# Optimization experiments

Measured on AMD Instinct MI355X. Metric: run time of the kernel, lower is better.

Reference implementation:

```python
import jax, jax.numpy as jnp
import numpy as np

NUM_TAGS = 128
BATCH = 512
SEQ = 512


def setup_inputs() -> dict:
    key = jax.random.key(0)
    k1, k2, k3, k4 = jax.random.split(key, 4)
    emissions = jax.random.normal(k1, (BATCH, SEQ, NUM_TAGS), dtype=jnp.float32)
    mask = jnp.ones((BATCH, SEQ), dtype=bool)
    start_transitions = jax.random.normal(k2, (NUM_TAGS,), dtype=jnp.float32)
    end_transitions = jax.random.normal(k3, (NUM_TAGS,), dtype=jnp.float32)
    transitions = jax.random.normal(k4, (NUM_TAGS, NUM_TAGS), dtype=jnp.float32)
    return {
        "emissions": emissions,
        "mask": mask,
        "start_transitions": start_transitions,
        "end_transitions": end_transitions,
        "transitions": transitions,
    }


def reference(emissions, mask, start_transitions, end_transitions, transitions):
    """Viterbi decode (max-plus DP + backtrace), vectorized over batch.

    Returns:
      paths:      [B, S] int32, best tag sequence; positions past seq_end are -1
      best_score: [B]    float32, Viterbi score of the best path
    """
    emissions = emissions.astype(jnp.float32)
    B, S, T = emissions.shape
    emis = jnp.swapaxes(emissions, 0, 1)   # [S, B, T]
    msk = jnp.swapaxes(mask, 0, 1)         # [S, B]

    # ---- forward max-plus recurrence ----
    score0 = start_transitions[None, :] + emis[0]        # [B, T]

    def fwd_step(score, xs):
        e_t, m_t = xs                                    # [B,T], [B]
        nxt = score[:, :, None] + transitions[None]      # [B, T_prev, T_next]
        best_score = jnp.max(nxt, axis=1) + e_t          # [B, T]
        best_tag = jnp.argmax(nxt, axis=1).astype(jnp.int32)  # [B, T]
        new_score = jnp.where(m_t[:, None], best_score, score)
        return new_score, best_tag

    score, history = jax.lax.scan(fwd_step, score0, (emis[1:], msk[1:]))
    # history: [S-1, B, T] backpointers for t = 1..S-1

    final = score + end_transitions[None, :]
    best_score = jnp.max(final, axis=1)                  # [B]
    best_last = jnp.argmax(final, axis=1).astype(jnp.int32)  # [B]

    seq_ends = jnp.sum(mask.astype(jnp.int32), axis=1) - 1   # [B]

    # ---- vectorized backtrace (reverse scan) ----
    def bwd_step(tag, xs):
        hist_t, t = xs                                   # [B,T], scalar
        path_t = tag                                     # tag at position t (valid if t <= seq_end)
        prev = jnp.take_along_axis(hist_t, tag[:, None], axis=1)[:, 0]
        tag = jnp.where(t <= seq_ends, prev, tag)
        return tag, path_t

    ts = jnp.arange(1, S)
    tag0, rev_paths = jax.lax.scan(bwd_step, best_last, (history, ts), reverse=True)
    paths = jnp.concatenate([tag0[:, None], jnp.swapaxes(rev_paths, 0, 1)], axis=1)  # [B,S]
    paths = jnp.where(mask, paths, -1)
    return paths, best_score
```

## Files before the change

kernel.cpp:

```cpp
#include <hip/hip_runtime.h>

#define NB 512
#define NS 512
#define NT 128

__global__ __launch_bounds__(512, 1)
void crf_viterbi_fast(const float* __restrict__ emis,
                      const float* __restrict__ start_t,
                      const float* __restrict__ end_t,
                      const float* __restrict__ trans,
                      float* __restrict__ out_paths,
                      float* __restrict__ out_score,
                      float* __restrict__ ws)
{
    __shared__ __align__(16) float scp[2][144];
    __shared__ float Tlds[NT * 129];
    __shared__ float finv[NT];
    __shared__ unsigned char pathb[NS];

    const int b   = blockIdx.x;
    const int tid = threadIdx.x;
    const int j   = tid >> 2;
    const int h   = tid & 3;

    for (int idx = tid; idx < NT * NT; idx += 512) {
        Tlds[(idx >> 7) * 129 + (idx & 127)] = trans[idx];
    }

    float tc[32];
    #pragma unroll
    for (int k = 0; k < 32; ++k) tc[k] = trans[(h * 32 + k) * NT + j];

    const float* eb   = emis + (size_t)b * NS * NT;
    float*       wrow = ws   + (size_t)b * NS * NT;

    const int jq = (j >> 5) * 36 + (j & 31);

    float ns = start_t[j] + eb[j];
    if (h == 0) { scp[0][jq] = ns; wrow[j] = ns; }
    __syncthreads();

    float e_next = eb[NT + j];
    int cur = 0;
    for (int t = 1; t < NS; ++t) {
        float e_cur = e_next;
        int tn = (t + 1 < NS) ? (t + 1) : (NS - 1);
        e_next = eb[(size_t)tn * NT + j];

        const float4* s4 = (const float4*)&scp[cur][h * 36];

        float m0, m1, m2, m3;
        {
            float4 A = s4[0];
            m0 = fmaxf(fmaxf(A.x + tc[0],  A.y + tc[1]),
                       fmaxf(A.z + tc[2],  A.w + tc[3]));
            A = s4[1];
            m0 = fmaxf(fmaxf(m0, A.x + tc[4]),  A.y + tc[5]);
            m0 = fmaxf(fmaxf(m0, A.z + tc[6]),  A.w + tc[7]);
            A = s4[2];
            m1 = fmaxf(fmaxf(A.x + tc[8],  A.y + tc[9]),
                       fmaxf(A.z + tc[10], A.w + tc[11]));
            A = s4[3];
            m1 = fmaxf(fmaxf(m1, A.x + tc[12]), A.y + tc[13]);
            m1 = fmaxf(fmaxf(m1, A.z + tc[14]), A.w + tc[15]);
            A = s4[4];
            m2 = fmaxf(fmaxf(A.x + tc[16], A.y + tc[17]),
                       fmaxf(A.z + tc[18], A.w + tc[19]));
            A = s4[5];
            m2 = fmaxf(fmaxf(m2, A.x + tc[20]), A.y + tc[21]);
            m2 = fmaxf(fmaxf(m2, A.z + tc[22]), A.w + tc[23]);
            A = s4[6];
            m3 = fmaxf(fmaxf(A.x + tc[24], A.y + tc[25]),
                       fmaxf(A.z + tc[26], A.w + tc[27]));
            A = s4[7];
            m3 = fmaxf(fmaxf(m3, A.x + tc[28]), A.y + tc[29]);
            m3 = fmaxf(fmaxf(m3, A.z + tc[30]), A.w + tc[31]);
        }
        float m = fmaxf(fmaxf(m0, m1), fmaxf(m2, m3));

        m = fmaxf(m, __shfl_xor(m, 1));
        m = fmaxf(m, __shfl_xor(m, 2));

        ns = m + e_cur;
        if (h == 0) {
            scp[cur ^ 1][jq] = ns;
            wrow[(size_t)t * NT + j] = ns;
        }
        __syncthreads();
        cur ^= 1;
    }

    float fin = ns + end_t[j];
    if (h == 0) finv[j] = fin;
    __syncthreads();

    if (tid < 64) {
        const int l = tid;

        float f0 = finv[l], f1 = finv[l + 64];
        float mv = fmaxf(f0, f1);
        mv = fmaxf(mv, __shfl_xor(mv, 1));
        mv = fmaxf(mv, __shfl_xor(mv, 2));
        mv = fmaxf(mv, __shfl_xor(mv, 4));
        mv = fmaxf(mv, __shfl_xor(mv, 8));
        mv = fmaxf(mv, __shfl_xor(mv, 16));
        mv = fmaxf(mv, __shfl_xor(mv, 32));
        unsigned long long b0 = __ballot(f0 == mv);
        unsigned long long b1 = __ballot(f1 == mv);
        int tag = b0 ? (int)__builtin_ctzll(b0) : 64 + (int)__builtin_ctzll(b1);
        if (l == 0) {
            out_score[b] = mv;
            pathb[NS - 1] = (unsigned char)tag;
        }

        const float* rp = wrow + (size_t)(NS - 2) * NT;
        float a0 = rp[l], a1 = rp[l + 64];

        for (int t = NS - 1; t >= 1; --t) {
            const float* rp2 = wrow + (size_t)(t >= 2 ? t - 2 : 0) * NT;
            float p0 = rp2[l], p1 = rp2[l + 64];

            float v0 = a0 + Tlds[l * 129 + tag];
            float v1 = a1 + Tlds[(l + 64) * 129 + tag];
            float m = fmaxf(v0, v1);
            m = fmaxf(m, __shfl_xor(m, 1));
            m = fmaxf(m, __shfl_xor(m, 2));
            m = fmaxf(m, __shfl_xor(m, 4));
            m = fmaxf(m, __shfl_xor(m, 8));
            m = fmaxf(m, __shfl_xor(m, 16));
            m = fmaxf(m, __shfl_xor(m, 32));
            unsigned long long c0 = __ballot(v0 == m);
            unsigned long long c1 = __ballot(v1 == m);
            tag = c0 ? (int)__builtin_ctzll(c0) : 64 + (int)__builtin_ctzll(c1);
            if (l == 0) pathb[t - 1] = (unsigned char)tag;

            a0 = p0; a1 = p1;
        }
    }
    __syncthreads();

    if (tid < NT) {
        float* op = out_paths + (size_t)b * NS;
        #pragma unroll
        for (int k = 0; k < NS / NT; ++k) {
            op[k * NT + tid] = (float)pathb[k * NT + tid];
        }
    }
}

__global__ __launch_bounds__(512, 1)
void crf_viterbi_fb(const float* __restrict__ emis,
                    const float* __restrict__ start_t,
                    const float* __restrict__ end_t,
                    const float* __restrict__ trans,
                    float* __restrict__ out_paths,
                    float* __restrict__ out_score)
{
    __shared__ __align__(16) float scp[2][144];
    __shared__ unsigned int histw[NS / 4][NT];
    __shared__ unsigned char pathb[NS];

    const int b   = blockIdx.x;
    const int tid = threadIdx.x;
    const int j   = tid >> 2;
    const int h   = tid & 3;

    float tc[32];
    #pragma unroll
    for (int k = 0; k < 32; ++k) tc[k] = trans[(h * 32 + k) * NT + j];

    const float* eb = emis + (size_t)b * NS * NT;
    const int jq = (j >> 5) * 36 + (j & 31);

    float ns = start_t[j] + eb[j];
    if (h == 0) scp[0][jq] = ns;
    __syncthreads();

    float e_next = eb[NT + j];
    unsigned int packed = 0;
    int cur = 0;
    for (int t = 1; t < NS; ++t) {
        float e_cur = e_next;
        int tn = (t + 1 < NS) ? (t + 1) : (NS - 1);
        e_next = eb[(size_t)tn * NT + j];

        const float4* s4 = (const float4*)&scp[cur][h * 36];
        float m0 = -INFINITY, m1 = -INFINITY;
        int x0 = 0, x1 = 0;
        #pragma unroll
        for (int q = 0; q < 4; ++q) {
            float4 A  = s4[q];
            float4 Bv = s4[4 + q];
            float v;
            v = A.x  + tc[4*q+0];     if (v > m0) { m0 = v; x0 = 4*q+0; }
            v = A.y  + tc[4*q+1];     if (v > m0) { m0 = v; x0 = 4*q+1; }
            v = A.z  + tc[4*q+2];     if (v > m0) { m0 = v; x0 = 4*q+2; }
            v = A.w  + tc[4*q+3];     if (v > m0) { m0 = v; x0 = 4*q+3; }
            v = Bv.x + tc[16+4*q+0];  if (v > m1) { m1 = v; x1 = 4*q+0; }
            v = Bv.y + tc[16+4*q+1];  if (v > m1) { m1 = v; x1 = 4*q+1; }
            v = Bv.z + tc[16+4*q+2];  if (v > m1) { m1 = v; x1 = 4*q+2; }
            v = Bv.w + tc[16+4*q+3];  if (v > m1) { m1 = v; x1 = 4*q+3; }
        }
        if (m1 > m0) { m0 = m1; x0 = x1 + 16; }
        float m = m0;
        int   x = h * 32 + x0;

        float mo = __shfl_xor(m, 1);
        int   xo = __shfl_xor(x, 1);
        float mlo = (h & 1) ? mo : m;  int xlo = (h & 1) ? xo : x;
        float mhi = (h & 1) ? m : mo;  int xhi = (h & 1) ? x : xo;
        if (mhi > mlo) { m = mhi; x = xhi; } else { m = mlo; x = xlo; }
        mo = __shfl_xor(m, 2);
        xo = __shfl_xor(x, 2);
        mlo = (h & 2) ? mo : m;  xlo = (h & 2) ? xo : x;
        mhi = (h & 2) ? m : mo;  xhi = (h & 2) ? x : xo;
        if (mhi > mlo) { m = mhi; x = xhi; } else { m = mlo; x = xlo; }

        ns = m + e_cur;
        packed |= (unsigned int)x << (8 * ((t - 1) & 3));
        if (h == 0) {
            if ((((t - 1) & 3) == 3) || (t == NS - 1))
                histw[(t - 1) >> 2][j] = packed;
            scp[cur ^ 1][jq] = ns;
        }
        if (((t - 1) & 3) == 3) packed = 0;
        __syncthreads();
        cur ^= 1;
    }

    float fin = ns + end_t[j];
    if (h == 0) scp[0][jq] = fin;
    __syncthreads();

    if (tid == 0) {
        float bm = scp[0][0]; int bi = 0;
        for (int i = 1; i < NT; ++i) {
            float v = scp[0][(i >> 5) * 36 + (i & 31)];
            if (v > bm) { bm = v; bi = i; }
        }
        out_score[b] = bm;
        int tag = bi;
        pathb[NS - 1] = (unsigned char)tag;
        for (int t = NS - 1; t >= 1; --t) {
            int idx = t - 1;
            unsigned int w = histw[idx >> 2][tag];
            tag = (int)((w >> (8 * (idx & 3))) & 0xFFu);
            pathb[t - 1] = (unsigned char)tag;
        }
    }
    __syncthreads();

    if (tid < NT) {
        float* op = out_paths + (size_t)b * NS;
        #pragma unroll
        for (int k = 0; k < NS / NT; ++k) {
            op[k * NT + tid] = (float)pathb[k * NT + tid];
        }
    }
}

extern "C" void kernel_launch(void* const* d_in, const int* in_sizes, int n_in,
                              void* d_out, int out_size, void* d_ws, size_t ws_size,
                              hipStream_t stream) {
    const float* emis    = (const float*)d_in[0];
    const float* start_t = (const float*)d_in[2];
    const float* end_t   = (const float*)d_in[3];
    const float* trans   = (const float*)d_in[4];

    float* paths = (float*)d_out;
    float* score = (float*)d_out + (size_t)NB * NS;

    const size_t need = (size_t)NB * NS * NT * sizeof(float);
    if (ws_size >= need) {
        crf_viterbi_fast<<<NB, 512, 0, stream>>>(emis, start_t, end_t, trans,
                                                 paths, score, (float*)d_ws);
    } else {
        crf_viterbi_fb<<<NB, 512, 0, stream>>>(emis, start_t, end_t, trans,
                                               paths, score);
    }
}
```

Baseline: 443.3 us.

## Store pre-emission max in workspace to skip backtrace max reduction; lighter LDS barrier

The forward pass now stores the max-plus result before adding the emission (m) instead of the full score, and the backtrace rebuilds the previous score as stored value plus emission. Because the stored max for the chosen tag is known, the backtrace compares candidates against that value directly and drops the six-step shuffle max reduction from its serial loop. This relies on the float sum being bit-identical between the two passes so the ballot equality finds the tag. The forward-loop barrier is also replaced with a waitcnt on LDS only plus s_barrier, so outstanding global stores are not waited on at each step.

New measurement: 419.1 us. -5.4%, faster.

```diff
diff --git a/kernel.cpp b/kernel.cpp
--- a/kernel.cpp
+++ b/kernel.cpp
@@ -3,6 +3,13 @@
 #define NB 512
 #define NS 512
 #define NT 128
+
+#define LDS_BARRIER()                                            \
+    do {                                                         \
+        asm volatile("s_waitcnt lgkmcnt(0)" ::: "memory");       \
+        __builtin_amdgcn_s_barrier();                            \
+        __builtin_amdgcn_sched_barrier(0);                       \
+    } while (0)
 
 __global__ __launch_bounds__(512, 1)
 void crf_viterbi_fast(const float* __restrict__ emis,
@@ -36,9 +43,10 @@
 
     const int jq = (j >> 5) * 36 + (j & 31);
 
-    float ns = start_t[j] + eb[j];
-    if (h == 0) { scp[0][jq] = ns; wrow[j] = ns; }
-    __syncthreads();
+    float st = start_t[j];
+    float ns = st + eb[j];
+    if (h == 0) { scp[0][jq] = ns; wrow[j] = st; }
+    LDS_BARRIER();
 
     float e_next = eb[NT + j];
     int cur = 0;
@@ -84,9 +92,9 @@
         ns = m + e_cur;
         if (h == 0) {
             scp[cur ^ 1][jq] = ns;
-            wrow[(size_t)t * NT + j] = ns;
-        }
-        __syncthreads();
+            wrow[(size_t)t * NT + j] = m;
+        }
+        LDS_BARRIER();
         cur ^= 1;
     }
 
@@ -113,28 +121,33 @@
             pathb[NS - 1] = (unsigned char)tag;
         }
 
-        const float* rp = wrow + (size_t)(NS - 2) * NT;
-        float a0 = rp[l], a1 = rp[l + 64];
+        float wM0 = wrow[(size_t)(NS - 1) * NT + l];
+        float wM1 = wrow[(size_t)(NS - 1) * NT + l + 64];
+        float cw0 = wrow[(size_t)(NS - 2) * NT + l];
+        float cw1 = wrow[(size_t)(NS - 2) * NT + l + 64];
+        float a0  = cw0 + eb[(size_t)(NS - 2) * NT + l];
+        float a1  = cw1 + eb[(size_t)(NS - 2) * NT + l + 64];
 
         for (int t = NS - 1; t >= 1; --t) {
-            const float* rp2 = wrow + (size_t)(t >= 2 ? t - 2 : 0) * NT;
-            float p0 = rp2[l], p1 = rp2[l + 64];
+            const int tp = (t >= 2) ? t - 2 : 0;
+            float pw0 = wrow[(size_t)tp * NT + l];
+            float pw1 = wrow[(size_t)tp * NT + l + 64];
+            float pe0 = eb[(size_t)tp * NT + l];
+            float pe1 = eb[(size_t)tp * NT + l + 64];
+
+            float wsel = (tag >= 64) ? wM1 : wM0;
+            float M = __shfl(wsel, tag & 63);
 
             float v0 = a0 + Tlds[l * 129 + tag];
             float v1 = a1 + Tlds[(l + 64) * 129 + tag];
-            float m = fmaxf(v0, v1);
-            m = fmaxf(m, __shfl_xor(m, 1));
-            m = fmaxf(m, __shfl_xor(m, 2));
-            m = fmaxf(m, __shfl_xor(m, 4));
-            m = fmaxf(m, __shfl_xor(m, 8));
-            m = fmaxf(m, __shfl_xor(m, 16));
-            m = fmaxf(m, __shfl_xor(m, 32));
-            unsigned long long c0 = __ballot(v0 == m);
-            unsigned long long c1 = __ballot(v1 == m);
+            unsigned long long c0 = __ballot(v0 == M);
+            unsigned long long c1 = __ballot(v1 == M);
             tag = c0 ? (int)__builtin_ctzll(c0) : 64 + (int)__builtin_ctzll(c1);
             if (l == 0) pathb[t - 1] = (unsigned char)tag;
 
-            a0 = p0; a1 = p1;
+            wM0 = cw0; wM1 = cw1;
+            a0 = pw0 + pe0; a1 = pw1 + pe1;
+            cw0 = pw0; cw1 = pw1;
         }
     }
     __syncthreads();
```
